# Optimization experiments

Measured on AMD Instinct MI355X. Metric: run time of the kernel, lower is better.

Reference implementation:

```python
import jax, jax.numpy as jnp
import numpy as np

N, S, M = 16, 256, 768
TK, HA = 10, 1          # tK stages, hA heads (from RTM.__init__)
DH = M // HA
EPS = 1e-5
WSCALE = 0.02           # scale on randn weights to keep 10 stacked stages numerically sane


def _pos_bias():
    # bias[i][j][z] = sin(j / 10000**(2z/M)), bias[i][j][z+1] = cos(...); independent of i
    pos = np.arange(S, dtype=np.float64)[:, None]
    z = np.arange(0, M, 2, dtype=np.float64)
    ang = pos / (10000.0 ** (2.0 * z / M))          # (S, M/2)
    pe = np.zeros((S, M), dtype=np.float32)
    pe[:, 0::2] = np.sin(ang)
    pe[:, 1::2] = np.cos(ang)
    return jnp.asarray(pe)

PE = _pos_bias()


def _ln(v, g, b):
    mu = jnp.mean(v, axis=-1, keepdims=True)
    var = jnp.var(v, axis=-1, keepdims=True)
    return (v - mu) / jnp.sqrt(var + EPS) * g + b


def setup_inputs() -> dict:
    key = jax.random.key(0)
    ks = jax.random.split(key, 8)
    rn = lambda k, shp: jax.random.normal(k, shp, dtype=jnp.float32)
    return {
        "x": rn(ks[0], (N, S, M)),
        "weight": rn(ks[1], (M, M)) * WSCALE,
        "Wq": rn(ks[2], (TK, HA, DH, M)) * WSCALE,
        "Wk": rn(ks[3], (TK, HA, DH, M)) * WSCALE,
        "Wv": rn(ks[4], (TK, HA, DH, M)) * WSCALE,
        "Wo": rn(ks[5], (TK, M, M)) * WSCALE,
        "ln1_g": jnp.ones((M,), jnp.float32), "ln1_b": jnp.zeros((M,), jnp.float32),
        "ln2_g": jnp.ones((M,), jnp.float32), "ln2_b": jnp.zeros((M,), jnp.float32),
        "fc1_w": rn(ks[6], (4 * M, M)) * WSCALE, "fc1_b": jnp.zeros((4 * M,), jnp.float32),
        "fc2_w": rn(ks[7], (M, 4 * M)) * WSCALE, "fc2_b": jnp.zeros((M,), jnp.float32),
    }


def reference(x, weight, Wq, Wk, Wv, Wo, ln1_g, ln1_b, ln2_g, ln2_b,
              fc1_w, fc1_b, fc2_w, fc2_b):
    # savespace[i,j] = weight @ x[i,j,:]  (x[j,:,i] after the double transpose), + sin/cos bias
    s0 = jnp.einsum('mn,ijn->ijm', weight, x) + PE[None, :, :]   # (N, S, M)
    inv_sqrt_dh = jnp.float32(1.0 / np.sqrt(DH))

    def mlp(s):
        h = jax.nn.gelu(s @ fc1_w.T + fc1_b, approximate=False)
        return h @ fc2_w.T + fc2_b

    # Sequential over tokens j: token j attends (strictly causal) to the per-stage V
    # of all previous tokens, accumulated in cumV. Within a token, the tK stages run
    # sequentially, each mutating the token's state s (as the torch code mutates savespace).
    def token_step(cumV, s):                # cumV: (TK, N, HA, DH); s: (N, M)
        newV = []
        for a in range(TK):
            sn = _ln(s, ln1_g, ln1_b)
            q = jnp.einsum('hdm,nm->nhd', Wq[a], sn)
            k = jnp.einsum('hdm,nm->nhd', Wk[a], sn)
            v = jnp.einsum('hdm,nm->nhd', Wv[a], sn)
            logit = jnp.sum(q * inv_sqrt_dh * k, axis=-1)                # (N, HA) scalar score
            rsa = jax.nn.softmax(logit[..., None], axis=-1)[..., 0]      # softmax of scalar == 1
            imv = cumV[a]                                                # (N, HA, DH): sum_{subj<j}
            s = jnp.einsum('mk,nk->nm', Wo[a], imv.reshape(N, HA * DH)) + s
            s = _ln(s, ln2_g, ln2_b) + s
            s = mlp(s)
            newV.append(rsa[..., None] * v)
        return cumV + jnp.stack(newV, axis=0), s

    cumV0 = jnp.zeros((TK, N, HA, DH), x.dtype)
    _, ys = jax.lax.scan(token_step, cumV0, jnp.swapaxes(s0, 0, 1))      # ys: (S, N, M)
    return jnp.swapaxes(ys, 0, 1)                                        # (N, S, M)
```

## Files before the change

kernel.cpp:

```cpp
#include <hip/hip_runtime.h>
#include <hip/hip_bf16.h>
#include <math.h>


using bf16   = __bf16;
using bf16x8 = __attribute__((ext_vector_type(8))) __bf16;
using f32x4  = __attribute__((ext_vector_type(4))) float;

#define DEV __device__ __forceinline__

DEV void gload16(const bf16* g, bf16* l) {
  __builtin_amdgcn_global_load_lds(
      (const __attribute__((address_space(1))) unsigned int*)g,
      (__attribute__((address_space(3))) unsigned int*)l, 16, 0, 0);
}

DEV float gelu_f(float x) {
  const float y  = x * 0.70710678118654752f;
  const float ay = fabsf(y);
  const float t  = __builtin_amdgcn_rcpf(__builtin_fmaf(0.3275911f, ay, 1.0f));
  float p = __builtin_fmaf(1.061405429f, t, -1.453152027f);
  p = __builtin_fmaf(p, t, 1.421413741f);
  p = __builtin_fmaf(p, t, -0.284496736f);
  p = __builtin_fmaf(p, t, 0.254829592f);
  p = p * t;
  const float e = __expf(-ay * ay);
  float er = __builtin_fmaf(-p, e, 1.0f);
  er = __builtin_copysignf(er, y);
  return 0.5f * x * (1.0f + er);
}

enum { EPI_PART = 0, EPI_GELU = 1, EPI_B16 = 2 };

template <int EPI>
__global__ __launch_bounds__(512, 2) void gemm256(
    const bf16* __restrict__ A, const bf16* __restrict__ B,
    float* __restrict__ outF, bf16* __restrict__ outB,
    const float* __restrict__ aux, int K, int N,
    int kZ, int klen, size_t oZ)
{
  constexpr int TBUF = 256 * 32;
  __shared__ bf16 As[4 * TBUF];
  __shared__ bf16 Bs[4 * TBUF];
  const int z = blockIdx.z;
  const int kbeg = z * kZ;
  const int tid = threadIdx.x, lane = tid & 63, w = tid >> 6;
  const int wr = w >> 2, wc = w & 3;

  const int nx = gridDim.x;
  const int nwg = nx * (int)gridDim.y;
  int f = blockIdx.x + nx * blockIdx.y;
  f = (f & 7) * (nwg >> 3) + (f >> 3);
  const int m0 = (f % nx) * 256, n0 = (f / nx) * 256;

  const int r  = tid >> 2;
  const int kq = ((tid & 3) - (tid >> 3)) & 3;
  const bf16* aG0 = A + (size_t)(m0 + r) * K + kq * 8 + kbeg;
  const bf16* aG1 = aG0 + (size_t)128 * K;
  const bf16* bG0 = B + (size_t)(n0 + r) * K + kq * 8 + kbeg;
  const bf16* bG1 = bG0 + (size_t)128 * K;

  const int lr = lane & 15, kb = lane >> 4;
  const int swz   = ((kb + (lr >> 1)) & 3) * 8;
  const int aBase = (wr * 128 + lr) * 32 + swz;
  const int bBase = (wc * 64 + lr) * 32 + swz;

  f32x4 acc[8][4] = {};
  const int NT = klen >> 5;

  auto stageA = [&](int buf, int t) {
    bf16* d = &As[buf * TBUF + tid * 8];
    gload16(aG0 + t * 32, d);
    gload16(aG1 + t * 32, d + 4096);
  };
  auto stageB = [&](int buf, int t) {
    bf16* d = &Bs[buf * TBUF + tid * 8];
    gload16(bG0 + t * 32, d);
    gload16(bG1 + t * 32, d + 4096);
  };

  stageA(0, 0); stageB(0, 0);
  if (NT > 1) { stageA(1, 1); stageB(1, 1); }
  if (NT > 2) { stageA(2, 2); stageB(2, 2); }
  if (NT > 2)      asm volatile("s_waitcnt vmcnt(8)" ::: "memory");
  else if (NT > 1) asm volatile("s_waitcnt vmcnt(4)" ::: "memory");
  else             asm volatile("s_waitcnt vmcnt(0)" ::: "memory");
  __builtin_amdgcn_s_barrier();
  asm volatile("" ::: "memory");

  for (int t = 0; t < NT; ++t) {
    const int pa = (t & 3) * TBUF;
    bf16x8 af[4], bfv[4];
#pragma unroll
    for (int g = 0; g < 4; ++g) af[g] = *(const bf16x8*)&As[pa + aBase + g * 512];
#pragma unroll
    for (int nt = 0; nt < 4; ++nt) bfv[nt] = *(const bf16x8*)&Bs[pa + bBase + nt * 512];
    if (t + 3 < NT) stageA((t + 3) & 3, t + 3);
    asm volatile("" ::: "memory");
    __builtin_amdgcn_s_barrier();
    asm volatile("" ::: "memory");
    __builtin_amdgcn_s_setprio(1);
#pragma unroll
    for (int g = 0; g < 4; ++g)
#pragma unroll
      for (int nt = 0; nt < 4; ++nt)
        acc[g][nt] = __builtin_amdgcn_mfma_f32_16x16x32_bf16(af[g], bfv[nt], acc[g][nt], 0, 0, 0);
    __builtin_amdgcn_s_setprio(0);
    asm volatile("" ::: "memory");
    __builtin_amdgcn_s_barrier();
    asm volatile("" ::: "memory");
#pragma unroll
    for (int g = 0; g < 4; ++g) af[g] = *(const bf16x8*)&As[pa + aBase + 2048 + g * 512];
    if (t + 3 < NT) stageB((t + 3) & 3, t + 3);
    asm volatile("" ::: "memory");
    __builtin_amdgcn_s_barrier();
    asm volatile("" ::: "memory");
    __builtin_amdgcn_s_setprio(1);
#pragma unroll
    for (int g = 0; g < 4; ++g)
#pragma unroll
      for (int nt = 0; nt < 4; ++nt)
        acc[4 + g][nt] = __builtin_amdgcn_mfma_f32_16x16x32_bf16(af[g], bfv[nt], acc[4 + g][nt], 0, 0, 0);
    __builtin_amdgcn_s_setprio(0);
    if (t + 3 < NT)      asm volatile("s_waitcnt vmcnt(8)" ::: "memory");
    else if (t + 2 < NT) asm volatile("s_waitcnt vmcnt(4)" ::: "memory");
    else if (t + 1 < NT) asm volatile("s_waitcnt vmcnt(0)" ::: "memory");
    asm volatile("" ::: "memory");
    __builtin_amdgcn_s_barrier();
    asm volatile("" ::: "memory");
  }

  const int row0 = m0 + wr * 128 + (lane >> 4) * 4;
  const int col0 = n0 + wc * 64 + lr;
  float* oF = (EPI == EPI_PART) ? outF + (size_t)z * oZ : nullptr;
#pragma unroll
  for (int mt = 0; mt < 8; ++mt) {
#pragma unroll
    for (int nt = 0; nt < 4; ++nt) {
      const int col = col0 + nt * 16;
      float bias = 0.f;
      if (EPI == EPI_GELU) bias = aux[col];
#pragma unroll
      for (int rg = 0; rg < 4; ++rg) {
        const int row = row0 + mt * 16 + rg;
        float v = acc[mt][nt][rg];
        if (EPI == EPI_PART) {
          oF[(size_t)row * N + col] = v;
        } else {
          outB[(size_t)row * N + col] = (bf16)gelu_f(v + bias);
        }
      }
    }
  }
}

template <int BN, int EPI>
__global__ __launch_bounds__(256) void gemm_k(
    const bf16* __restrict__ A, const bf16* __restrict__ B,
    float* __restrict__ outF, bf16* __restrict__ outB,
    const float* __restrict__ aux, int K, int N,
    int kZ, int klen, size_t aZ, size_t bZ, size_t oZ)
{
  constexpr int ABUF = 128 * 32;
  constexpr int BBUF = BN * 32;
  __shared__ bf16 As[3 * ABUF];
  __shared__ bf16 Bs[3 * BBUF];
  const int z = blockIdx.z;
  A += (size_t)z * aZ;
  B += (size_t)z * bZ;
  const int kbeg = z * kZ;
  const int tid  = threadIdx.x;
  const int lane = tid & 63, wave = tid >> 6;
  const int m0 = blockIdx.x * 128, n0 = blockIdx.y * BN;

  const int r  = tid >> 2;
  const int kq = ((tid & 3) - (tid >> 3)) & 3;
  const bf16* aG0 = A + (size_t)(m0 + r) * K + kq * 8 + kbeg;
  const bf16* aG1 = aG0 + (size_t)64 * K;
  const bf16* bG0 = B + (size_t)(n0 + r) * K + kq * 8 + kbeg;
  const bf16* bG1 = bG0 + (size_t)64 * K;

  const int wr = (wave & 1) * 64, wc = (wave >> 1) * (BN / 2);
  const int lr = lane & 15, kb = lane >> 4;
  const int swz  = ((kb + (lr >> 1)) & 3) * 8;
  const int aOff = (wr + lr) * 32 + swz;
  const int bOff = (wc + lr) * 32 + swz;

  constexpr int MT = 4, NT = BN / 32;
  f32x4 acc[MT][NT] = {};
  const int iters = klen >> 5;

  auto stage = [&](int p, int k0) {
    bf16* aD = &As[p * ABUF + tid * 8];
    gload16(aG0 + k0, aD);
    gload16(aG1 + k0, aD + 2048);
    bf16* bD = &Bs[p * BBUF + tid * 8];
    gload16(bG0 + k0, bD);
    if (BN == 128) gload16(bG1 + k0, bD + 2048);
  };

  stage(0, 0);
  if (iters > 1) stage(1, 32);
  int cur = 0, nxt = 2;
  for (int it = 0; it < iters; ++it) {
    if (it + 1 < iters) {
      if constexpr (BN == 128) asm volatile("s_waitcnt vmcnt(4)" ::: "memory");
      else                     asm volatile("s_waitcnt vmcnt(3)" ::: "memory");
    } else {
      asm volatile("s_waitcnt vmcnt(0)" ::: "memory");
    }
    __builtin_amdgcn_s_barrier();
    asm volatile("" ::: "memory");
    if (it + 2 < iters) stage(nxt, (it + 2) * 32);
    asm volatile("" ::: "memory");
    const int pa = cur * ABUF, pb = cur * BBUF;
    bf16x8 af[MT], bfv[NT];
#pragma unroll
    for (int t = 0; t < MT; ++t) af[t] = *(const bf16x8*)&As[pa + aOff + t * 512];
#pragma unroll
    for (int t = 0; t < NT; ++t) bfv[t] = *(const bf16x8*)&Bs[pb + bOff + t * 512];
#pragma unroll
    for (int mt = 0; mt < MT; ++mt)
#pragma unroll
      for (int nt = 0; nt < NT; ++nt)
        acc[mt][nt] = __builtin_amdgcn_mfma_f32_16x16x32_bf16(af[mt], bfv[nt], acc[mt][nt], 0, 0, 0);
    cur = (cur == 2) ? 0 : cur + 1;
    nxt = (nxt == 2) ? 0 : nxt + 1;
  }

  const int row0 = m0 + wr + (lane >> 4) * 4;
  const int col0 = n0 + wc + lr;
  float* oF = (EPI == EPI_PART) ? outF + (size_t)z * oZ : nullptr;
  bf16*  oB = (EPI == EPI_B16)  ? outB + (size_t)z * oZ : outB;
#pragma unroll
  for (int mt = 0; mt < MT; ++mt) {
#pragma unroll
    for (int nt = 0; nt < NT; ++nt) {
      const int col = col0 + nt * 16;
      float bias = 0.f;
      if (EPI == EPI_GELU) bias = aux[col];
#pragma unroll
      for (int rg = 0; rg < 4; ++rg) {
        const int row = row0 + mt * 16 + rg;
        float v = acc[mt][nt][rg];
        if (EPI == EPI_PART) {
          oF[(size_t)row * N + col] = v;
        } else if (EPI == EPI_GELU) {
          oB[(size_t)row * N + col] = (bf16)gelu_f(v + bias);
        } else {
          oB[(size_t)row * N + col] = (bf16)v;
        }
      }
    }
  }
}

template <int NP, int MODE>
__global__ __launch_bounds__(256) void reduce_ln(
    const float* __restrict__ P, size_t pZ,
    const float* __restrict__ add, const float* __restrict__ g,
    const float* __restrict__ b, float* __restrict__ Tout,
    bf16* __restrict__ SNout)
{
  const int row = blockIdx.x, t = threadIdx.x;
  float v[3];
#pragma unroll
  for (int c = 0; c < 3; ++c) {
    const int col = t + c * 256;
    float s = P[(size_t)row * 768 + col];
#pragma unroll
    for (int p = 1; p < NP; ++p) s += P[(size_t)p * pZ + (size_t)row * 768 + col];
    if (MODE == 0) s += add[(row & 255) * 768 + col];
    if (MODE == 1) s += add[(size_t)row * 768 + col];
    if (MODE == 2 || MODE == 3) s += add[col];
    v[c] = s;
  }
  if (MODE != 1) {
#pragma unroll
    for (int c = 0; c < 3; ++c) Tout[(size_t)row * 768 + t + c * 256] = v[c];
  }
  if (MODE == 3) return;

  __shared__ float red[8];
  float s = v[0] + v[1] + v[2];
#pragma unroll
  for (int o = 32; o >= 1; o >>= 1) s += __shfl_down(s, o);
  if ((t & 63) == 0) red[t >> 6] = s;
  __syncthreads();
  const float mu = (red[0] + red[1] + red[2] + red[3]) * (1.f / 768.f);
  const float d0 = v[0] - mu, d1 = v[1] - mu, d2 = v[2] - mu;
  float q = d0 * d0 + d1 * d1 + d2 * d2;
#pragma unroll
  for (int o = 32; o >= 1; o >>= 1) q += __shfl_down(q, o);
  if ((t & 63) == 0) red[4 + (t >> 6)] = q;
  __syncthreads();
  const float var = (red[4] + red[5] + red[6] + red[7]) * (1.f / 768.f);
  const float rs = rsqrtf(var + 1e-5f);
  float y0 = d0 * rs * g[t] + b[t];
  float y1 = d1 * rs * g[t + 256] + b[t + 256];
  float y2 = d2 * rs * g[t + 512] + b[t + 512];
  if (MODE == 1) { y0 += v[0]; y1 += v[1]; y2 += v[2]; }
  bf16* o = SNout + (size_t)row * 768;
  o[t] = (bf16)y0; o[t + 256] = (bf16)y1; o[t + 512] = (bf16)y2;
}

__global__ __launch_bounds__(256) void scan_partial_b(
    const bf16* __restrict__ SN, float* __restrict__ Ps)
{
  const int n = blockIdx.x, ch = blockIdx.y, d = blockIdx.z * 256 + threadIdx.x;
  const bf16* base = SN + ((size_t)(n * 256 + ch * 16)) * 768 + d;
  float s = 0.f;
#pragma unroll
  for (int j = 0; j < 16; ++j) s += (float)base[(size_t)j * 768];
  Ps[(size_t)(n * 16 + ch) * 768 + d] = s;
}

__global__ __launch_bounds__(256) void scan_final_b(
    const bf16* __restrict__ SN, const float* __restrict__ Ps,
    bf16* __restrict__ PSb)
{
  const int n = blockIdx.x, ch = blockIdx.y, d = blockIdx.z * 256 + threadIdx.x;
  float run = 0.f;
  for (int c = 0; c < ch; ++c) run += Ps[(size_t)(n * 16 + c) * 768 + d];
  const bf16* vb = SN + ((size_t)(n * 256 + ch * 16)) * 768 + d;
  bf16* ob = PSb + ((size_t)(n * 256 + ch * 16)) * 768 + d;
#pragma unroll
  for (int j = 0; j < 16; ++j) {
    ob[(size_t)j * 768] = (bf16)run;
    run += (float)vb[(size_t)j * 768];
  }
}

__global__ __launch_bounds__(256) void transpose_wv(
    const float* __restrict__ Wv, bf16* __restrict__ WvT)
{
  __shared__ float tile[64][65];
  const int a = blockIdx.z, k0 = blockIdx.x * 64, n0 = blockIdx.y * 64;
  const int c = threadIdx.x & 63, r4 = threadIdx.x >> 6;
  const float* src = Wv + (size_t)a * 589824;
  bf16* dst = WvT + (size_t)a * 589824;
#pragma unroll
  for (int i = 0; i < 16; ++i)
    tile[r4 + i * 4][c] = src[(size_t)(k0 + r4 + i * 4) * 768 + n0 + c];
  __syncthreads();
#pragma unroll
  for (int i = 0; i < 16; ++i) {
    const int n = r4 + i * 4;
    dst[(size_t)(n0 + n) * 768 + k0 + c] = (bf16)tile[c][n];
  }
}

__global__ __launch_bounds__(256) void f32_to_bf16_k(
    const float* __restrict__ in, bf16* __restrict__ out, int n4)
{
  const int i = blockIdx.x * 256 + threadIdx.x;
  if (i >= n4) return;
  const float4 v = ((const float4*)in)[i];
  bf16 h[4] = {(bf16)v.x, (bf16)v.y, (bf16)v.z, (bf16)v.w};
  *(uint2*)(out + 4 * (size_t)i) = *(uint2*)h;
}

__global__ __launch_bounds__(256) void pe_kernel(float* __restrict__ PE)
{
  const int id = blockIdx.x * 256 + threadIdx.x;
  const int j = id / 384, p = id % 384;
  const double ang = (double)j * pow(10000.0, -4.0 * (double)p / 768.0);
  PE[(size_t)j * 768 + 2 * p]     = (float)sin(ang);
  PE[(size_t)j * 768 + 2 * p + 1] = (float)cos(ang);
}

extern "C" void kernel_launch(void* const* d_in, const int* in_sizes, int n_in,
                              void* d_out, int out_size, void* d_ws, size_t ws_size,
                              hipStream_t stream)
{
  const float* x      = (const float*)d_in[0];
  const float* weight = (const float*)d_in[1];
  const float* Wv     = (const float*)d_in[4];
  const float* Wo     = (const float*)d_in[5];
  const float* ln1g   = (const float*)d_in[6];
  const float* ln1b   = (const float*)d_in[7];
  const float* ln2g   = (const float*)d_in[8];
  const float* ln2b   = (const float*)d_in[9];
  const float* fc1w   = (const float*)d_in[10];
  const float* fc1b   = (const float*)d_in[11];
  const float* fc2w   = (const float*)d_in[12];
  const float* fc2b   = (const float*)d_in[13];
  float* out = (float*)d_out;

  char* p = (char*)d_ws;
  auto alloc = [&](size_t bytes) { char* r = p; p += (bytes + 255) & ~(size_t)255; return r; };
  bf16*  Wb_w  = (bf16*)alloc(589824ull * 2);
  bf16*  Wb_o  = (bf16*)alloc(5898240ull * 2);
  bf16*  WvT   = (bf16*)alloc(5898240ull * 2);
  bf16*  Wvo   = (bf16*)alloc(5898240ull * 2);
  bf16*  Wb_f1 = (bf16*)alloc(2359296ull * 2);
  bf16*  Wb_f2 = (bf16*)alloc(2359296ull * 2);
  bf16*  Xb    = (bf16*)alloc(3145728ull * 2);
  float* PEf   = (float*)alloc(196608ull * 4);
  float* T     = (float*)alloc(3145728ull * 4);
  bf16*  SN    = (bf16*)alloc(3145728ull * 2);
  bf16*  PSb   = (bf16*)alloc(3145728ull * 2);
  bf16*  H     = (bf16*)alloc(12582912ull * 2);
  float* Ps    = (float*)alloc(196608ull * 4);
  float* Part  = (float*)alloc(4ull * 3145728ull * 4);

  auto cvt = [&](const float* src, bf16* dst, int n) {
    int n4 = n / 4;
    f32_to_bf16_k<<<(n4 + 255) / 256, 256, 0, stream>>>(src, dst, n4);
  };
  cvt(x, Xb, 3145728);
  cvt(weight, Wb_w, 589824);
  cvt(Wo, Wb_o, 5898240);
  cvt(fc1w, Wb_f1, 2359296);
  cvt(fc2w, Wb_f2, 2359296);
  transpose_wv<<<dim3(12, 12, 10), 256, 0, stream>>>(Wv, WvT);
  pe_kernel<<<384, 256, 0, stream>>>(PEf);

  gemm_k<128, EPI_B16><<<dim3(6, 6, 10), 256, 0, stream>>>(
      Wb_o, WvT, nullptr, Wvo, nullptr, 768, 768, 0, 768, 589824, 589824, 589824);

  gemm_k<64, EPI_PART><<<dim3(32, 12, 2), 256, 0, stream>>>(
      Xb, Wb_w, Part, nullptr, nullptr, 768, 768, 384, 384, 0, 0, 3145728);
  reduce_ln<2, 0><<<4096, 256, 0, stream>>>(Part, 3145728, PEf, ln1g, ln1b, T, SN);

  for (int a = 0; a < 10; ++a) {
    scan_partial_b<<<dim3(16, 16, 3), 256, 0, stream>>>(SN, Ps);
    scan_final_b<<<dim3(16, 16, 3), 256, 0, stream>>>(SN, Ps, PSb);
    gemm_k<64, EPI_PART><<<dim3(32, 12, 2), 256, 0, stream>>>(
        PSb, Wvo + (size_t)a * 589824, Part, nullptr, nullptr, 768, 768, 384, 384, 0, 0, 3145728);
    reduce_ln<2, 1><<<4096, 256, 0, stream>>>(Part, 3145728, T, ln2g, ln2b, nullptr, SN);
    gemm256<EPI_GELU><<<dim3(16, 12, 1), 512, 0, stream>>>(
        SN, Wb_f1, nullptr, H, fc1b, 768, 3072, 0, 768, 0);
    gemm256<EPI_PART><<<dim3(16, 3, 4), 512, 0, stream>>>(
        H, Wb_f2, Part, nullptr, nullptr, 3072, 768, 768, 768, 3145728);
    if (a < 9)
      reduce_ln<4, 2><<<4096, 256, 0, stream>>>(Part, 3145728, fc2b, ln1g, ln1b, T, SN);
    else
      reduce_ln<4, 3><<<4096, 256, 0, stream>>>(Part, 3145728, fc2b, nullptr, nullptr, out, nullptr);
  }
  (void)in_sizes; (void)n_in; (void)out_size; (void)ws_size;
}
```

Before: 1.369 ms.

## Simplify gemm_k to double buffering and route fc2 through gemm_k split-K 2

The gemm_k main loop goes from a three-buffer LDS pipeline with explicit partial vmcnt waits to a two-buffer pipeline guarded by __syncthreads each iteration. The fc2 GEMM moves from the 256-tile gemm256 kernel with 4-way split-K to gemm_k with 128x64 tiles and 2-way split-K. The partial-sum buffer and the following reductions shrink from 4 slices to 2. This cuts LDS use and partial-sum traffic, but it risks less load/compute overlap in every gemm_k call and a less efficient tile shape for the large-K fc2 GEMM.

```diff
diff --git a/kernel.cpp b/kernel.cpp
--- a/kernel.cpp
+++ b/kernel.cpp
@@ -163,8 +163,8 @@
 {
   constexpr int ABUF = 128 * 32;
   constexpr int BBUF = BN * 32;
-  __shared__ bf16 As[3 * ABUF];
-  __shared__ bf16 Bs[3 * BBUF];
+  __shared__ bf16 Asl[2 * ABUF];
+  __shared__ bf16 Bsl[2 * BBUF];
   const int z = blockIdx.z;
   A += (size_t)z * aZ;
   B += (size_t)z * bZ;
@@ -186,46 +186,34 @@
   const int aOff = (wr + lr) * 32 + swz;
   const int bOff = (wc + lr) * 32 + swz;
 
-  constexpr int MT = 4, NT = BN / 32;
-  f32x4 acc[MT][NT] = {};
+  constexpr int MT = 4, NTT = BN / 32;
+  f32x4 acc[MT][NTT] = {};
   const int iters = klen >> 5;
 
   auto stage = [&](int p, int k0) {
-    bf16* aD = &As[p * ABUF + tid * 8];
+    bf16* aD = &Asl[p * ABUF + tid * 8];
     gload16(aG0 + k0, aD);
     gload16(aG1 + k0, aD + 2048);
-    bf16* bD = &Bs[p * BBUF + tid * 8];
+    bf16* bD = &Bsl[p * BBUF + tid * 8];
     gload16(bG0 + k0, bD);
     if (BN == 128) gload16(bG1 + k0, bD + 2048);
   };
 
   stage(0, 0);
-  if (iters > 1) stage(1, 32);
-  int cur = 0, nxt = 2;
   for (int it = 0; it < iters; ++it) {
-    if (it + 1 < iters) {
-      if constexpr (BN == 128) asm volatile("s_waitcnt vmcnt(4)" ::: "memory");
-      else                     asm volatile("s_waitcnt vmcnt(3)" ::: "memory");
-    } else {
-      asm volatile("s_waitcnt vmcnt(0)" ::: "memory");
-    }
-    __builtin_amdgcn_s_barrier();
-    asm volatile("" ::: "memory");
-    if (it + 2 < iters) stage(nxt, (it + 2) * 32);
-    asm volatile("" ::: "memory");
-    const int pa = cur * ABUF, pb = cur * BBUF;
-    bf16x8 af[MT], bfv[NT];
-#pragma unroll
-    for (int t = 0; t < MT; ++t) af[t] = *(const bf16x8*)&As[pa + aOff + t * 512];
-#pragma unroll
-    for (int t = 0; t < NT; ++t) bfv[t] = *(const bf16x8*)&Bs[pb + bOff + t * 512];
+    __syncthreads();
+    if (it + 1 < iters) stage((it + 1) & 1, (it + 1) * 32);
+    const int pa = (it & 1) * ABUF, pb = (it & 1) * BBUF;
+    bf16x8 af[MT], bfv[NTT];
+#pragma unroll
+    for (int t = 0; t < MT; ++t) af[t] = *(const bf16x8*)&Asl[pa + aOff + t * 512];
+#pragma unroll
+    for (int t = 0; t < NTT; ++t) bfv[t] = *(const bf16x8*)&Bsl[pb + bOff + t * 512];
 #pragma unroll
     for (int mt = 0; mt < MT; ++mt)
 #pragma unroll
-      for (int nt = 0; nt < NT; ++nt)
+      for (int nt = 0; nt < NTT; ++nt)
         acc[mt][nt] = __builtin_amdgcn_mfma_f32_16x16x32_bf16(af[mt], bfv[nt], acc[mt][nt], 0, 0, 0);
-    cur = (cur == 2) ? 0 : cur + 1;
-    nxt = (nxt == 2) ? 0 : nxt + 1;
   }
 
   const int row0 = m0 + wr + (lane >> 4) * 4;
@@ -235,7 +223,7 @@
 #pragma unroll
   for (int mt = 0; mt < MT; ++mt) {
 #pragma unroll
-    for (int nt = 0; nt < NT; ++nt) {
+    for (int nt = 0; nt < NTT; ++nt) {
       const int col = col0 + nt * 16;
       float bias = 0.f;
       if (EPI == EPI_GELU) bias = aux[col];
@@ -402,7 +390,7 @@
   bf16*  PSb   = (bf16*)alloc(3145728ull * 2);
   bf16*  H     = (bf16*)alloc(12582912ull * 2);
   float* Ps    = (float*)alloc(196608ull * 4);
-  float* Part  = (float*)alloc(4ull * 3145728ull * 4);
+  float* Part  = (float*)alloc(2ull * 3145728ull * 4);
 
   auto cvt = [&](const float* src, bf16* dst, int n) {
     int n4 = n / 4;
@@ -431,12 +419,12 @@
     reduce_ln<2, 1><<<4096, 256, 0, stream>>>(Part, 3145728, T, ln2g, ln2b, nullptr, SN);
     gemm256<EPI_GELU><<<dim3(16, 12, 1), 512, 0, stream>>>(
         SN, Wb_f1, nullptr, H, fc1b, 768, 3072, 0, 768, 0);
-    gemm256<EPI_PART><<<dim3(16, 3, 4), 512, 0, stream>>>(
-        H, Wb_f2, Part, nullptr, nullptr, 3072, 768, 768, 768, 3145728);
+    gemm_k<64, EPI_PART><<<dim3(32, 12, 2), 256, 0, stream>>>(
+        H, Wb_f2, Part, nullptr, nullptr, 3072, 768, 1536, 1536, 0, 0, 3145728);
     if (a < 9)
-      reduce_ln<4, 2><<<4096, 256, 0, stream>>>(Part, 3145728, fc2b, ln1g, ln1b, T, SN);
+      reduce_ln<2, 2><<<4096, 256, 0, stream>>>(Part, 3145728, fc2b, ln1g, ln1b, T, SN);
     else
-      reduce_ln<4, 3><<<4096, 256, 0, stream>>>(Part, 3145728, fc2b, nullptr, nullptr, out, nullptr);
+      reduce_ln<2, 3><<<4096, 256, 0, stream>>>(Part, 3145728, fc2b, nullptr, nullptr, out, nullptr);
   }
   (void)in_sizes; (void)n_in; (void)out_size; (void)ws_size;
 }
```

After: 1.319 ms. 3.6% less time.
